# Kernel tuning notes

Hardware: AMD Instinct MI355X
Metric: run time of the kernel (lower is better)

The kernel has to match this reference:

```python
import jax, jax.numpy as jnp
import numpy as np

B, M, N, K = 2, 25000, 100000, 16
HID, DIM, NGROUPS = 64, 64, 8
GN_EPS = 1e-5


def conv1x1(x, w, b):
    # x: [B,C,M,K], w: [O,C], b: [O]
    return jnp.einsum('bcmk,oc->bomk', x, w) + b[None, :, None, None]


def group_norm(x, gamma, beta, ngroups):
    b, c, m, k = x.shape
    xg = x.reshape(b, ngroups, c // ngroups, m, k)
    mu = xg.mean(axis=(2, 3, 4), keepdims=True)
    var = xg.var(axis=(2, 3, 4), keepdims=True)
    xn = ((xg - mu) / jnp.sqrt(var + GN_EPS)).reshape(b, c, m, k)
    return xn * gamma[None, :, None, None] + beta[None, :, None, None]


def mlp(x, w1, b1, g, be, w2, b2):
    h = jax.nn.relu(group_norm(conv1x1(x, w1, b1), g, be, NGROUPS))
    return conv1x1(h, w2, b2)


def setup_inputs() -> dict:
    key = jax.random.key(0)
    ks = jax.random.split(key, 16)
    inp = {
        'q_xyzs': jax.random.normal(ks[0], (B, 3, M), jnp.float32),
        'k_xyzs': jax.random.normal(ks[1], (B, 3, N), jnp.float32),
        'knn_idx': jax.random.randint(ks[2], (B, M, K), 0, N),
        'mask': jax.random.randint(ks[3], (B, M, K), 0, 2).astype(bool),
        # embed_positions MLP params
        'pe_w1': jax.random.normal(ks[4], (HID, 4), jnp.float32) * 0.05,
        'pe_b1': jnp.zeros((HID,), jnp.float32),
        'pe_g': jnp.ones((HID,), jnp.float32),
        'pe_be': jnp.zeros((HID,), jnp.float32),
        'pe_w2': jax.random.normal(ks[5], (DIM, HID), jnp.float32) * 0.05,
        'pe_b2': jnp.zeros((DIM,), jnp.float32),
        # attention MLP params
        'at_w1': jax.random.normal(ks[6], (HID, DIM), jnp.float32) * 0.05,
        'at_b1': jnp.zeros((HID,), jnp.float32),
        'at_g': jnp.ones((HID,), jnp.float32),
        'at_be': jnp.zeros((HID,), jnp.float32),
        'at_w2': jax.random.normal(ks[7], (DIM, HID), jnp.float32) * 0.05,
        'at_b2': jnp.zeros((DIM,), jnp.float32),
    }
    return inp


def reference(q_xyzs, k_xyzs, knn_idx, mask,
              pe_w1, pe_b1, pe_g, pe_be, pe_w2, pe_b2,
              at_w1, at_b1, at_g, at_be, at_w2, at_b2):
    # gather KNN coordinates: [B,3,M,K]
    knn_xyzs = jax.vmap(lambda pts, idx: pts[:, idx])(k_xyzs, knn_idx)
    offset = knn_xyzs - q_xyzs[..., None]
    dist = jnp.linalg.norm(offset, axis=1, keepdims=True)  # [B,1,M,K]
    direction = offset / jnp.maximum(dist, 1e-12)
    local_pattern = jnp.concatenate([direction, dist], axis=1)  # [B,4,M,K]

    pe = mlp(local_pattern, pe_w1, pe_b1, pe_g, pe_be, pe_w2, pe_b2)  # [B,DIM,M,K]
    attn = mlp(pe, at_w1, at_b1, at_g, at_be, at_w2, at_b2)
    mask_value = -jnp.finfo(attn.dtype).max
    attn = jnp.where(mask[:, None], attn, mask_value)
    attn = jax.nn.softmax(attn, axis=-1)
    return (pe * attn).sum(axis=-1)  # [B,DIM,M]
```

## Files before the change

kernel.cpp:

```cpp
#include <hip/hip_runtime.h>

#define Bn 2
#define Mn 25000
#define Nn 100000
#define MK 400000
#define GN_EPS 1e-5f
#define NEG_BIG (-3.402823466e+38f)
#define LOG2E 1.44269504088896340736f
#define MASK_NEG (-60000.f)

#define G1 512
#define G2 512

#define BEFF_OFF 0
#define B1P_OFF  64
#define AB1P_OFF 192
#define AB2L_OFF 320
#define WF16_OFF 384
#define AW1P_OFF 6528
#define W1F_OFF  10624
#define MSK_OFF  11136
#define SP_OFF   36160
#define YP_OFF   52544
#define YS_OFF   183616
#define KXT_OFF  184128
#define QT_OFF   984128
#define XF_OFF   1184128

typedef _Float16 hf8 __attribute__((ext_vector_type(8)));
typedef _Float16 hf4 __attribute__((ext_vector_type(4)));
typedef _Float16 hf2 __attribute__((ext_vector_type(2)));
typedef float f32x16 __attribute__((ext_vector_type(16)));

__device__ __forceinline__ f32x16 mfma16(hf8 a, hf8 b, f32x16 c) {
    return __builtin_amdgcn_mfma_f32_32x32x16_f16(a, b, c, 0, 0, 0);
}
__device__ __forceinline__ f32x16 splat16(float v) {
    f32x16 x;
#pragma unroll
    for (int r = 0; r < 16; ++r) x[r] = v;
    return x;
}
__device__ __forceinline__ hf8 zero8() {
    hf8 z;
#pragma unroll
    for (int j = 0; j < 8; ++j) z[j] = (_Float16)0.f;
    return z;
}
__device__ __forceinline__ hf2 pkcvt(float a, float b) {
    return __builtin_bit_cast(hf2, __builtin_amdgcn_cvt_pkrtz(a, b));
}
__device__ __forceinline__ hf2 pkrelu(hf2 v) {
    hf2 z; z[0] = (_Float16)0.f; z[1] = (_Float16)0.f;
    return __builtin_elementwise_max(v, z);
}
__device__ __forceinline__ float waveSum(float v) {
#pragma unroll
    for (int s = 32; s; s >>= 1) v += __shfl_down(v, s, 64);
    return v;
}
#define ROWFN(r, lane) (((r) & 3) + 8*((r) >> 2) + 4*((lane) >> 5))
#define SWZH(row, col) ((col) ^ ((((row) & 7)) << 3))

__global__ __launch_bounds__(256) void prep0_kernel(
    const float* __restrict__ q, const float* __restrict__ kx,
    float* __restrict__ ws)
{
    float4* kxt = (float4*)(ws + KXT_OFF);
    float4* qt  = (float4*)(ws + QT_OFF);
    for (int e = blockIdx.x*256 + threadIdx.x; e < 2*Nn; e += gridDim.x*256) {
        const int b = e / Nn, n = e % Nn;
        float4 v;
        v.x = kx[(b*3+0)*Nn + n]; v.y = kx[(b*3+1)*Nn + n];
        v.z = kx[(b*3+2)*Nn + n]; v.w = 0.f;
        kxt[e] = v;
    }
    for (int e = blockIdx.x*256 + threadIdx.x; e < 2*Mn; e += gridDim.x*256) {
        const int b = e / Mn, m = e % Mn;
        float4 v;
        v.x = q[(b*3+0)*Mn + m]; v.y = q[(b*3+1)*Mn + m];
        v.z = q[(b*3+2)*Mn + m]; v.w = 0.f;
        qt[e] = v;
    }
}

__global__ __launch_bounds__(256) void gatherx_kernel(
    const int* __restrict__ idx, const int* __restrict__ mask,
    float* __restrict__ ws)
{
    __shared__ float red[4][16];
    const int b = blockIdx.y;
    const float4* kxt = (const float4*)(ws + KXT_OFF) + (size_t)b*Nn;
    const float4* qt  = (const float4*)(ws + QT_OFF)  + (size_t)b*Mn;
    _Float16* xf = (_Float16*)(ws + XF_OFF);
    unsigned short* m16 = (unsigned short*)(ws + MSK_OFF) + (size_t)b*25024;
    float v[14];
#pragma unroll
    for (int j = 0; j < 14; ++j) v[j] = 0.f;

    for (int i = blockIdx.x*256 + threadIdx.x; i < MK; i += G1*256) {
        const int mm = i >> 4;
        const int id = idx[(size_t)b*MK + i];
        const float4 kv = kxt[id];
        const float4 qv = qt[mm];
        const float ox = kv.x - qv.x, oy = kv.y - qv.y, oz = kv.z - qv.z;
        const float d  = sqrtf(ox*ox + oy*oy + oz*oz);
        const float inv = 1.0f / fmaxf(d, 1e-12f);
        const float x0 = ox*inv, x1 = oy*inv, x2 = oz*inv, x3 = d;

        const hf2 lo = pkcvt(x0, x1);
        const hf2 hi = pkcvt(x2, x3);
        hf4 pk;
        pk[0] = lo[0]; pk[1] = lo[1]; pk[2] = hi[0]; pk[3] = hi[1];
        *(hf4*)&xf[((size_t)b*MK + i)*4] = pk;

        const unsigned long long mb = __ballot(mask[(size_t)b*MK + i] != 0);
        if ((threadIdx.x & 63) == 0)
            *(unsigned long long*)&m16[i >> 4] = mb;

        v[0] += x0; v[1] += x1; v[2] += x2; v[3] += x3;
        v[4] += x0*x0; v[5] += x0*x1; v[6] += x0*x2; v[7] += x0*x3;
        v[8] += x1*x1; v[9] += x1*x2; v[10] += x1*x3;
        v[11] += x2*x2; v[12] += x2*x3; v[13] += x3*x3;
    }
    const int lane = threadIdx.x & 63, wv = threadIdx.x >> 6;
#pragma unroll
    for (int j = 0; j < 14; ++j) v[j] = waveSum(v[j]);
    if (lane == 0) {
#pragma unroll
        for (int j = 0; j < 14; ++j) red[wv][j] = v[j];
    }
    __syncthreads();
    if (threadIdx.x < 14)
        ws[SP_OFF + ((size_t)b*G1 + blockIdx.x)*16 + threadIdx.x] =
            red[0][threadIdx.x] + red[1][threadIdx.x] + red[2][threadIdx.x] + red[3][threadIdx.x];
}

__global__ void prep1_kernel(
    const float* __restrict__ ws_r,
    const float* __restrict__ w1, const float* __restrict__ b1,
    const float* __restrict__ g1, const float* __restrict__ be1,
    const float* __restrict__ w2, const float* __restrict__ pe_b2,
    const float* __restrict__ aw1, const float* __restrict__ ab1,
    const float* __restrict__ aw2, const float* __restrict__ ab2,
    float* __restrict__ ws)
{
    const int t = threadIdx.x;
    _Float16* WF = (_Float16*)(ws + WF16_OFF);

    if (blockIdx.x > 0) {
        const int e = (blockIdx.x - 1)*256 + t;
        const int o = e >> 6, c = e & 63;
        WF[e]        = (_Float16)w2[e];
        WF[4096 + e] = (_Float16)(aw2[e] * LOG2E);
        float acc = 0.f;
        for (int d = 0; d < 64; ++d) acc = fmaf(aw1[o*64 + d], w2[d*64 + c], acc);
        WF[8192 + e] = (_Float16)acc;
        return;
    }

    __shared__ double S[2][14];
    __shared__ double Sp[28][8];
    __shared__ float Eh[2][64], Eq[2][64];

    if (t < 224) {
        const int p = t >> 3, sub = t & 7;
        const int b = p / 14, j = p % 14;
        const float* src = ws_r + SP_OFF + (size_t)b*G1*16 + j;
        double acc = 0.0;
        for (int g = sub; g < G1; g += 8)
            acc += (double)src[(size_t)g*16];
        Sp[p][sub] = acc;
    }
    __syncthreads();
    if (t < 28) {
        double acc = 0.0;
#pragma unroll
        for (int s = 0; s < 8; ++s) acc += Sp[t][s];
        S[t / 14][t % 14] = acc;
    }
    __syncthreads();

    if (t < 128) {
        const int b = t >> 6, o = t & 63;
        const double inv = 1.0 / (double)MK;
        double mu[4];
#pragma unroll
        for (int c = 0; c < 4; ++c) mu[c] = S[b][c] * inv;
        double m2[4][4];
        {
            const int map[4][4] = {{0,1,2,3},{1,4,5,6},{2,5,7,8},{3,6,8,9}};
#pragma unroll
            for (int c = 0; c < 4; ++c)
#pragma unroll
                for (int c2 = 0; c2 < 4; ++c2)
                    m2[c][c2] = S[b][4 + map[c][c2]] * inv;
        }
        double w[4];
#pragma unroll
        for (int c = 0; c < 4; ++c) w[c] = (double)w1[o*4 + c];
        double s = 0.0, qd = 0.0;
#pragma unroll
        for (int c = 0; c < 4; ++c) {
            s += w[c] * mu[c];
#pragma unroll
            for (int c2 = 0; c2 < 4; ++c2) qd += w[c]*w[c2]*m2[c][c2];
        }
        const double bb = (double)b1[o];
        Eh[b][o] = (float)(s + bb);
        Eq[b][o] = (float)(qd + 2.0*bb*s + bb*bb);
    }
    __syncthreads();
    if (t < 128) {
        const int b = t >> 6, o = t & 63, g = o & ~7;
        float mg = 0.f, qg = 0.f;
#pragma unroll
        for (int j = 0; j < 8; ++j) { mg += Eh[b][g + j]; qg += Eq[b][g + j]; }
        mg *= 0.125f; qg *= 0.125f;
        const float var = fmaxf(qg - mg*mg, 0.f);
        const float a = g1[o] / sqrtf(var + GN_EPS);
        const float c1v = be1[o] - mg*a;
        _Float16* W1F = (_Float16*)(ws + W1F_OFF);
        hf8 wrow;
#pragma unroll
        for (int c = 0; c < 4; ++c) wrow[c] = (_Float16)(a * w1[o*4 + c]);
#pragma unroll
        for (int c = 4; c < 8; ++c) wrow[c] = (_Float16)0.f;
        *(hf8*)&W1F[(b*64 + o)*8] = wrow;
        ws[B1P_OFF + b*64 + o] = fmaf(a, b1[o], c1v);
    }
    if (t < 64) {
        float acc = ab1[t];
        for (int d = 0; d < 64; ++d) acc = fmaf(aw1[t*64 + d], pe_b2[d], acc);
        ws[BEFF_OFF + t] = acc;
    } else if (t < 128) {
        ws[AB2L_OFF + (t - 64)] = ab2[t - 64] * LOG2E;
    }
}

__global__ __launch_bounds__(256, 4) void pass2_kernel(
    const float* __restrict__ cws, float* __restrict__ ws)
{
    __shared__ __align__(16) _Float16 Xs[4][32][72];
    const int b = blockIdx.y;
    const int tid = threadIdx.x, lane = tid & 63, wv = tid >> 6;
    const int colA = lane & 31;
    const int klo = (lane >> 5) * 8;
    const _Float16* xf  = (const _Float16*)(cws + XF_OFF);
    const _Float16* WFe = (const _Float16*)(cws + WF16_OFF) + 8192;
    const _Float16* W1F = (const _Float16*)(cws + W1F_OFF);

    hf8 BW[2][4];
#pragma unroll
    for (int jc = 0; jc < 2; ++jc)
#pragma unroll
        for (int ks = 0; ks < 4; ++ks)
            BW[jc][ks] = *(const hf8*)&WFe[(2*colA + jc)*64 + 16*ks + klo];
    hf8 BX[2];
    if (klo == 0) {
        BX[0] = *(const hf8*)&W1F[(b*64 + 2*colA)*8];
        BX[1] = *(const hf8*)&W1F[(b*64 + 2*colA + 1)*8];
    } else { BX[0] = zero8(); BX[1] = zero8(); }
    const float bias0 = cws[B1P_OFF + b*64 + 2*colA];
    const float bias1 = cws[B1P_OFF + b*64 + 2*colA + 1];

    float sh[2] = {0.f, 0.f}, sq[2] = {0.f, 0.f};

    for (int base = blockIdx.x * 128; base < MK; base += G2 * 128) {
        const int pt0 = base + 32*wv;
        hf8 ax = zero8();
        if (klo == 0) {
            hf4 xv = *(const hf4*)&xf[((size_t)b*MK + pt0 + colA)*4];
#pragma unroll
            for (int j = 0; j < 4; ++j) ax[j] = xv[j];
        }
        f32x16 r0 = splat16(bias0), r1t = splat16(bias1);
        r0  = mfma16(ax, BX[0], r0);
        r1t = mfma16(ax, BX[1], r1t);
#pragma unroll
        for (int r = 0; r < 16; ++r) {
            const int row = ROWFN(r, lane);
            *(hf2*)&Xs[wv][row][2*colA] = pkrelu(pkcvt(r0[r], r1t[r]));
        }
        hf8 A[4];
#pragma unroll
        for (int ks = 0; ks < 4; ++ks)
            A[ks] = *(const hf8*)&Xs[wv][colA][16*ks + klo];
#pragma unroll
        for (int jc = 0; jc < 2; ++jc) {
            f32x16 C = splat16(0.f);
#pragma unroll
            for (int ks = 0; ks < 4; ++ks) C = mfma16(A[ks], BW[jc][ks], C);
#pragma unroll
            for (int r = 0; r < 16; ++r) {
                const float vy = C[r];
                sh[jc] += vy;
                sq[jc] = fmaf(vy, vy, sq[jc]);
            }
        }
    }

#pragma unroll
    for (int jc = 0; jc < 2; ++jc) {
        sh[jc] += __shfl_xor(sh[jc], 32, 64);
        sq[jc] += __shfl_xor(sq[jc], 32, 64);
    }
    __syncthreads();
    float* red = (float*)Xs;
    if (lane < 32) {
#pragma unroll
        for (int jc = 0; jc < 2; ++jc) {
            red[wv*128 +      2*colA + jc] = sh[jc];
            red[wv*128 + 64 + 2*colA + jc] = sq[jc];
        }
    }
    __syncthreads();
    if (tid < 128) {
        const float v = red[tid] + red[128 + tid] + red[256 + tid] + red[384 + tid];
        ws[YP_OFF + ((size_t)b*G2 + blockIdx.x)*128 + tid] = v;
    }
}

__global__ __launch_bounds__(64) void prep2a_kernel(
    const float* __restrict__ ws_r, float* __restrict__ ws)
{
    const int o2 = blockIdx.x;
    const int b = o2 >> 7, i = o2 & 127;
    const float* p = ws_r + YP_OFF + (size_t)b*G2*128 + i;
    double acc = 0.0;
    for (int g = threadIdx.x; g < G2; g += 64) acc += (double)p[(size_t)g*128];
#pragma unroll
    for (int s = 32; s; s >>= 1) acc += __shfl_down(acc, s, 64);
    if (threadIdx.x == 0) ((double*)(ws + YS_OFF))[o2] = acc;
}

__global__ void prep2b_kernel(const float* __restrict__ ws_r,
                              const float* __restrict__ g2, const float* __restrict__ be2,
                              const float* __restrict__ aw1, const float* __restrict__ ab1,
                              float* __restrict__ ws)
{
    __shared__ float EH[2][64], EQ[2][64];
    __shared__ float A2s[2][64];
    const int t = threadIdx.x;
    const double* YS = (const double*)(ws_r + YS_OFF);
    if (t < 128) {
        const int b = t >> 6, o = t & 63;
        const double invMK = 1.0 / (double)MK;
        const double my = YS[b*128 + o] * invMK;
        const double qy = YS[b*128 + 64 + o] * invMK;
        const double beff = (double)ws_r[BEFF_OFF + o];
        EH[b][o] = (float)(my + beff);
        EQ[b][o] = (float)(qy + 2.0*beff*my + beff*beff);
    }
    __syncthreads();
    if (t < 128) {
        const int b = t >> 6, o = t & 63, g = o & ~7;
        float mg = 0.f, qg = 0.f;
#pragma unroll
        for (int j = 0; j < 8; ++j) { mg += EH[b][g + j]; qg += EQ[b][g + j]; }
        mg *= 0.125f; qg *= 0.125f;
        const float var = fmaxf(qg - mg*mg, 0.f);
        const float a = g2[o] / sqrtf(var + GN_EPS);
        A2s[b][o] = a;
        ws[AB1P_OFF + b*64 + o] = fmaf(a, ab1[o], be2[o] - mg*a);
    }
    __syncthreads();
    _Float16* AW1P = (_Float16*)(ws + AW1P_OFF);
    for (int e = t; e < 8192; e += 256) {
        const int b = e >> 12, oc = e & 4095, o = oc >> 6;
        AW1P[e] = (_Float16)(A2s[b][o] * aw1[oc]);
    }
}

__global__ __launch_bounds__(256, 5) void pass3_kernel(
    const float* __restrict__ b2,
    const float* __restrict__ cws, float* __restrict__ out)
{
    __shared__ __align__(16) _Float16 Xs[8][32][64];
    float* O = (float*)Xs;

    const int b = blockIdx.y;
    const int base = blockIdx.x * 256;
    const int tid = threadIdx.x;
    const int lane = tid & 63, wv = tid >> 6;
    const int colA = lane & 31;
    const int hi = lane >> 5;
    const int klo = hi * 8;

    const _Float16* xf   = (const _Float16*)(cws + XF_OFF);
    const _Float16* WF   = (const _Float16*)(cws + WF16_OFF);
    const _Float16* AW1P = (const _Float16*)(cws + AW1P_OFF) + (size_t)b*4096;
    const _Float16* W1F  = (const _Float16*)(cws + W1F_OFF);
    const unsigned short* m16 = (const unsigned short*)(cws + MSK_OFF) + (size_t)b*25024;

    int pt0[2];
    pt0[0] = base + 64*wv;
    pt0[1] = base + 64*wv + 32;
    unsigned mb[2];
#pragma unroll
    for (int t = 0; t < 2; ++t)
        mb[t] = (pt0[t] < MK) ? *(const unsigned*)(m16 + (pt0[t] >> 4)) : 0u;
    const unsigned mbs0 = __builtin_amdgcn_readfirstlane(mb[0]);
    const unsigned mbs1 = __builtin_amdgcn_readfirstlane(mb[1]);

    {
        hf8 BX0, BX1;
        if (klo == 0) {
            BX0 = *(const hf8*)&W1F[(b*64 + 2*colA)*8];
            BX1 = *(const hf8*)&W1F[(b*64 + 2*colA + 1)*8];
        } else { BX0 = zero8(); BX1 = zero8(); }
        const float bias0 = cws[B1P_OFF + b*64 + 2*colA];
        const float bias1 = cws[B1P_OFF + b*64 + 2*colA + 1];
#pragma unroll
        for (int t = 0; t < 2; ++t) {
            hf8 ax = zero8();
            if (klo == 0 && pt0[t] < MK) {
                hf4 xv = *(const hf4*)&xf[((size_t)b*MK + pt0[t] + colA)*4];
#pragma unroll
                for (int j = 0; j < 4; ++j) ax[j] = xv[j];
            }
            f32x16 r0 = splat16(bias0), r1t = splat16(bias1);
            r0  = mfma16(ax, BX0, r0);
            r1t = mfma16(ax, BX1, r1t);
#pragma unroll
            for (int r = 0; r < 16; ++r) {
                const int row = ROWFN(r, lane);
                *(hf2*)&Xs[2*wv + t][row][SWZH(row, 2*colA)] = pkrelu(pkcvt(r0[r], r1t[r]));
            }
        }
    }

    hf2 pe_pk[2][16];
    {
        f32x16 p00 = splat16(b2[2*colA]);
        f32x16 p01 = splat16(b2[2*colA + 1]);
        f32x16 p10 = p00, p11 = p01;
#pragma unroll
        for (int ks = 0; ks < 4; ++ks) {
            const int off = SWZH(colA, 16*ks + klo);
            hf8 a0  = *(const hf8*)&Xs[2*wv    ][colA][off];
            hf8 a1  = *(const hf8*)&Xs[2*wv + 1][colA][off];
            hf8 b0f = *(const hf8*)&WF[(2*colA)*64 + 16*ks + klo];
            hf8 b1f = *(const hf8*)&WF[(2*colA + 1)*64 + 16*ks + klo];
            p00 = mfma16(a0, b0f, p00);
            p01 = mfma16(a0, b1f, p01);
            p10 = mfma16(a1, b0f, p10);
            p11 = mfma16(a1, b1f, p11);
        }
#pragma unroll
        for (int r = 0; r < 16; ++r) {
            const int row = ROWFN(r, lane);
            pe_pk[0][r] = pkcvt(p00[r], p01[r]);
            pe_pk[1][r] = pkcvt(p10[r], p11[r]);
            *(hf2*)&Xs[2*wv    ][row][SWZH(row, 2*colA)] = pe_pk[0][r];
            *(hf2*)&Xs[2*wv + 1][row][SWZH(row, 2*colA)] = pe_pk[1][r];
        }
    }

    {
        f32x16 h00 = splat16(cws[AB1P_OFF + b*64 + 2*colA]);
        f32x16 h01 = splat16(cws[AB1P_OFF + b*64 + 2*colA + 1]);
        f32x16 h10 = h00, h11 = h01;
#pragma unroll
        for (int ks = 0; ks < 4; ++ks) {
            const int off = SWZH(colA, 16*ks + klo);
            hf8 a0  = *(const hf8*)&Xs[2*wv    ][colA][off];
            hf8 a1  = *(const hf8*)&Xs[2*wv + 1][colA][off];
            hf8 b0f = *(const hf8*)&AW1P[(2*colA)*64 + 16*ks + klo];
            hf8 b1f = *(const hf8*)&AW1P[(2*colA + 1)*64 + 16*ks + klo];
            h00 = mfma16(a0, b0f, h00);
            h01 = mfma16(a0, b1f, h01);
            h10 = mfma16(a1, b0f, h10);
            h11 = mfma16(a1, b1f, h11);
        }
#pragma unroll
        for (int r = 0; r < 16; ++r) {
            const int row = ROWFN(r, lane);
            *(hf2*)&Xs[2*wv    ][row][SWZH(row, 2*colA)] = pkrelu(pkcvt(h00[r], h01[r]));
            *(hf2*)&Xs[2*wv + 1][row][SWZH(row, 2*colA)] = pkrelu(pkcvt(h10[r], h11[r]));
        }
    }

    f32x16 l00 = splat16(cws[AB2L_OFF + 2*colA]);
    f32x16 l01 = splat16(cws[AB2L_OFF + 2*colA + 1]);
    f32x16 l10 = l00, l11 = l01;
#pragma unroll
    for (int ks = 0; ks < 4; ++ks) {
        const int off = SWZH(colA, 16*ks + klo);
        hf8 a0  = *(const hf8*)&Xs[2*wv    ][colA][off];
        hf8 a1  = *(const hf8*)&Xs[2*wv + 1][colA][off];
        hf8 b0f = *(const hf8*)&WF[4096 + (2*colA)*64 + 16*ks + klo];
        hf8 b1f = *(const hf8*)&WF[4096 + (2*colA + 1)*64 + 16*ks + klo];
        l00 = mfma16(a0, b0f, l00);
        l01 = mfma16(a0, b1f, l01);
        l10 = mfma16(a1, b0f, l10);
        l11 = mfma16(a1, b1f, l11);
    }

    {
        const unsigned msh0 = mbs0 >> (4*hi);
        const unsigned msh1 = mbs1 >> (4*hi);
#pragma unroll
        for (int r = 0; r < 16; ++r) {
            const int bit = (r & 3) + 8*(r >> 2);
            const bool k0 = (msh0 >> bit) & 1u;
            const bool k1 = (msh1 >> bit) & 1u;
            l00[r] = k0 ? l00[r] : MASK_NEG;
            l01[r] = k0 ? l01[r] : MASK_NEG;
            l10[r] = k1 ? l10[r] : MASK_NEG;
            l11[r] = k1 ? l11[r] : MASK_NEG;
        }
    }

    __syncthreads();

    {
        auto softmax_tile = [&](const f32x16& lg, const hf2* pp, unsigned mbst,
                                int t, int j) {
#pragma unroll
            for (int mh = 0; mh < 2; ++mh) {
                float mx = lg[8*mh];
#pragma unroll
                for (int rr = 1; rr < 8; ++rr) mx = fmaxf(mx, lg[8*mh + rr]);
                mx = fmaxf(mx, __shfl_xor(mx, 32, 64));
                float se, sw = 0.f;
                if (((mbst >> (16*mh)) & 0xFFFFu) != 0u) {
                    se = 0.f;
#pragma unroll
                    for (int rr = 0; rr < 8; ++rr) {
                        const float e = exp2f(lg[8*mh + rr] - mx);
                        se += e;
                        sw = fmaf(e, (float)pp[8*mh + rr][j], sw);
                    }
                } else {
                    se = 8.f;
#pragma unroll
                    for (int rr = 0; rr < 8; ++rr) sw += (float)pp[8*mh + rr][j];
                }
                se += __shfl_xor(se, 32, 64);
                sw += __shfl_xor(sw, 32, 64);
                if (lane < 32)
                    O[(2*lane + j)*17 + (4*wv + 2*t + mh)] = sw * __builtin_amdgcn_rcpf(se);
            }
        };
        softmax_tile(l00, pe_pk[0], mbs0, 0, 0);
        softmax_tile(l01, pe_pk[0], mbs0, 0, 1);
        softmax_tile(l10, pe_pk[1], mbs1, 1, 0);
        softmax_tile(l11, pe_pk[1], mbs1, 1, 1);
    }
    __syncthreads();

    {
        const int o = tid >> 2, mq = (tid & 3) * 4;
        const int m0 = blockIdx.x * 16;
        if (m0 + mq < Mn) {
            float4 v;
            v.x = O[o*17 + mq];     v.y = O[o*17 + mq + 1];
            v.z = O[o*17 + mq + 2]; v.w = O[o*17 + mq + 3];
            *(float4*)&out[((size_t)b*64 + o)*Mn + m0 + mq] = v;
        }
    }
}

extern "C" void kernel_launch(void* const* d_in, const int* in_sizes, int n_in,
                              void* d_out, int out_size, void* d_ws, size_t ws_size,
                              hipStream_t stream) {
    (void)in_sizes; (void)n_in; (void)out_size; (void)ws_size;
    const float* q    = (const float*)d_in[0];
    const float* kx   = (const float*)d_in[1];
    const int*   idx  = (const int*)  d_in[2];
    const int*   mask = (const int*)  d_in[3];
    const float* w1   = (const float*)d_in[4];
    const float* b1   = (const float*)d_in[5];
    const float* g1   = (const float*)d_in[6];
    const float* be1  = (const float*)d_in[7];
    const float* w2   = (const float*)d_in[8];
    const float* b2   = (const float*)d_in[9];
    const float* aw1  = (const float*)d_in[10];
    const float* ab1  = (const float*)d_in[11];
    const float* g2   = (const float*)d_in[12];
    const float* be2  = (const float*)d_in[13];
    const float* aw2  = (const float*)d_in[14];
    const float* ab2  = (const float*)d_in[15];
    float* out = (float*)d_out;
    float* ws  = (float*)d_ws;

    prep0_kernel<<<256, 256, 0, stream>>>(q, kx, ws);
    gatherx_kernel<<<dim3(G1, Bn), 256, 0, stream>>>(idx, mask, ws);
    prep1_kernel<<<17, 256, 0, stream>>>(ws, w1, b1, g1, be1, w2, b2, aw1, ab1, aw2, ab2, ws);
    pass2_kernel<<<dim3(G2, Bn), 256, 0, stream>>>(ws, ws);
    prep2a_kernel<<<256, 64, 0, stream>>>(ws, ws);
    prep2b_kernel<<<1, 256, 0, stream>>>(ws, g2, be2, aw1, ab1, ws);
    pass3_kernel<<<dim3((MK + 255)/256, Bn), 256, 0, stream>>>(b2, ws, out);
}
```

Baseline: 220.8 us.

## Unroll gather loop by two, pad LDS rows instead of XOR swizzle

The gather kernel now processes two strided elements per iteration, loading both indices, masks and coordinate vectors before computing, to raise memory-level parallelism on the random kxt gather. In pass3, the XOR-swizzled LDS layout is replaced by padding each row to 72 halves, which simplifies address math. The launch-bounds minimum-blocks hint drops from 5 to 3, giving the compiler more registers per thread. The padding raises shared memory per block, and the lower occupancy hint may reduce latency hiding in pass3.

```diff
diff --git a/kernel.cpp b/kernel.cpp
--- a/kernel.cpp
+++ b/kernel.cpp
@@ -60,7 +60,6 @@
     return v;
 }
 #define ROWFN(r, lane) (((r) & 3) + 8*((r) >> 2) + 4*((lane) >> 5))
-#define SWZH(row, col) ((col) ^ ((((row) & 7)) << 3))
 
 __global__ __launch_bounds__(256) void prep0_kernel(
     const float* __restrict__ q, const float* __restrict__ kx,
@@ -98,23 +97,19 @@
 #pragma unroll
     for (int j = 0; j < 14; ++j) v[j] = 0.f;
 
-    for (int i = blockIdx.x*256 + threadIdx.x; i < MK; i += G1*256) {
-        const int mm = i >> 4;
-        const int id = idx[(size_t)b*MK + i];
-        const float4 kv = kxt[id];
-        const float4 qv = qt[mm];
+    auto process = [&](int i, const float4 kv, const float4 qv, int mk) {
         const float ox = kv.x - qv.x, oy = kv.y - qv.y, oz = kv.z - qv.z;
         const float d  = sqrtf(ox*ox + oy*oy + oz*oz);
         const float inv = 1.0f / fmaxf(d, 1e-12f);
         const float x0 = ox*inv, x1 = oy*inv, x2 = oz*inv, x3 = d;
 
         const hf2 lo = pkcvt(x0, x1);
-        const hf2 hi = pkcvt(x2, x3);
+        const hf2 h2 = pkcvt(x2, x3);
         hf4 pk;
-        pk[0] = lo[0]; pk[1] = lo[1]; pk[2] = hi[0]; pk[3] = hi[1];
+        pk[0] = lo[0]; pk[1] = lo[1]; pk[2] = h2[0]; pk[3] = h2[1];
         *(hf4*)&xf[((size_t)b*MK + i)*4] = pk;
 
-        const unsigned long long mb = __ballot(mask[(size_t)b*MK + i] != 0);
+        const unsigned long long mb = __ballot(mk != 0);
         if ((threadIdx.x & 63) == 0)
             *(unsigned long long*)&m16[i >> 4] = mb;
 
@@ -122,7 +117,31 @@
         v[4] += x0*x0; v[5] += x0*x1; v[6] += x0*x2; v[7] += x0*x3;
         v[8] += x1*x1; v[9] += x1*x2; v[10] += x1*x3;
         v[11] += x2*x2; v[12] += x2*x3; v[13] += x3*x3;
-    }
+    };
+
+    const int stride = G1*256;
+    int i = blockIdx.x*256 + threadIdx.x;
+    for (; i + stride < MK; i += 2*stride) {
+        const int iB = i + stride;
+        const int idA = idx[(size_t)b*MK + i];
+        const int idB = idx[(size_t)b*MK + iB];
+        const int mA  = mask[(size_t)b*MK + i];
+        const int mB  = mask[(size_t)b*MK + iB];
+        const float4 kvA = kxt[idA];
+        const float4 kvB = kxt[idB];
+        const float4 qvA = qt[i >> 4];
+        const float4 qvB = qt[iB >> 4];
+        process(i,  kvA, qvA, mA);
+        process(iB, kvB, qvB, mB);
+    }
+    for (; i < MK; i += stride) {
+        const int id = idx[(size_t)b*MK + i];
+        const int mk = mask[(size_t)b*MK + i];
+        const float4 kv = kxt[id];
+        const float4 qv = qt[i >> 4];
+        process(i, kv, qv, mk);
+    }
+
     const int lane = threadIdx.x & 63, wv = threadIdx.x >> 6;
 #pragma unroll
     for (int j = 0; j < 14; ++j) v[j] = waveSum(v[j]);
@@ -372,11 +391,11 @@
     }
 }
 
-__global__ __launch_bounds__(256, 5) void pass3_kernel(
+__global__ __launch_bounds__(256, 3) void pass3_kernel(
     const float* __restrict__ b2,
     const float* __restrict__ cws, float* __restrict__ out)
 {
-    __shared__ __align__(16) _Float16 Xs[8][32][64];
+    __shared__ __align__(16) _Float16 Xs[8][32][72];
     float* O = (float*)Xs;
 
     const int b = blockIdx.y;
@@ -425,7 +444,7 @@
 #pragma unroll
             for (int r = 0; r < 16; ++r) {
                 const int row = ROWFN(r, lane);
-                *(hf2*)&Xs[2*wv + t][row][SWZH(row, 2*colA)] = pkrelu(pkcvt(r0[r], r1t[r]));
+                *(hf2*)&Xs[2*wv + t][row][2*colA] = pkrelu(pkcvt(r0[r], r1t[r]));
             }
         }
     }
@@ -437,11 +456,11 @@
         f32x16 p10 = p00, p11 = p01;
 #pragma unroll
         for (int ks = 0; ks < 4; ++ks) {
-            const int off = SWZH(colA, 16*ks + klo);
+            const int off = 16*ks + klo;
             hf8 a0  = *(const hf8*)&Xs[2*wv    ][colA][off];
             hf8 a1  = *(const hf8*)&Xs[2*wv + 1][colA][off];
-            hf8 b0f = *(const hf8*)&WF[(2*colA)*64 + 16*ks + klo];
-            hf8 b1f = *(const hf8*)&WF[(2*colA + 1)*64 + 16*ks + klo];
+            hf8 b0f = *(const hf8*)&WF[(2*colA)*64 + off];
+            hf8 b1f = *(const hf8*)&WF[(2*colA + 1)*64 + off];
             p00 = mfma16(a0, b0f, p00);
             p01 = mfma16(a0, b1f, p01);
             p10 = mfma16(a1, b0f, p10);
@@ -452,8 +471,8 @@
             const int row = ROWFN(r, lane);
             pe_pk[0][r] = pkcvt(p00[r], p01[r]);
             pe_pk[1][r] = pkcvt(p10[r], p11[r]);
-            *(hf2*)&Xs[2*wv    ][row][SWZH(row, 2*colA)] = pe_pk[0][r];
-            *(hf2*)&Xs[2*wv + 1][row][SWZH(row, 2*colA)] = pe_pk[1][r];
+            *(hf2*)&Xs[2*wv    ][row][2*colA] = pe_pk[0][r];
+            *(hf2*)&Xs[2*wv + 1][row][2*colA] = pe_pk[1][r];
         }
     }
 
@@ -463,11 +482,11 @@
         f32x16 h10 = h00, h11 = h01;
 #pragma unroll
         for (int ks = 0; ks < 4; ++ks) {
-            const int off = SWZH(colA, 16*ks + klo);
+            const int off = 16*ks + klo;
             hf8 a0  = *(const hf8*)&Xs[2*wv    ][colA][off];
             hf8 a1  = *(const hf8*)&Xs[2*wv + 1][colA][off];
-            hf8 b0f = *(const hf8*)&AW1P[(2*colA)*64 + 16*ks + klo];
-            hf8 b1f = *(const hf8*)&AW1P[(2*colA + 1)*64 + 16*ks + klo];
+            hf8 b0f = *(const hf8*)&AW1P[(2*colA)*64 + off];
+            hf8 b1f = *(const hf8*)&AW1P[(2*colA + 1)*64 + off];
             h00 = mfma16(a0, b0f, h00);
             h01 = mfma16(a0, b1f, h01);
             h10 = mfma16(a1, b0f, h10);
@@ -476,8 +495,8 @@
 #pragma unroll
         for (int r = 0; r < 16; ++r) {
             const int row = ROWFN(r, lane);
-            *(hf2*)&Xs[2*wv    ][row][SWZH(row, 2*colA)] = pkrelu(pkcvt(h00[r], h01[r]));
-            *(hf2*)&Xs[2*wv + 1][row][SWZH(row, 2*colA)] = pkrelu(pkcvt(h10[r], h11[r]));
+            *(hf2*)&Xs[2*wv    ][row][2*colA] = pkrelu(pkcvt(h00[r], h01[r]));
+            *(hf2*)&Xs[2*wv + 1][row][2*colA] = pkrelu(pkcvt(h10[r], h11[r]));
         }
     }
 
@@ -486,11 +505,11 @@
     f32x16 l10 = l00, l11 = l01;
 #pragma unroll
     for (int ks = 0; ks < 4; ++ks) {
-        const int off = SWZH(colA, 16*ks + klo);
+        const int off = 16*ks + klo;
         hf8 a0  = *(const hf8*)&Xs[2*wv    ][colA][off];
         hf8 a1  = *(const hf8*)&Xs[2*wv + 1][colA][off];
-        hf8 b0f = *(const hf8*)&WF[4096 + (2*colA)*64 + 16*ks + klo];
-        hf8 b1f = *(const hf8*)&WF[4096 + (2*colA + 1)*64 + 16*ks + klo];
+        hf8 b0f = *(const hf8*)&WF[4096 + (2*colA)*64 + off];
+        hf8 b1f = *(const hf8*)&WF[4096 + (2*colA + 1)*64 + off];
         l00 = mfma16(a0, b0f, l00);
         l01 = mfma16(a0, b1f, l01);
         l10 = mfma16(a1, b0f, l10);
```

Result: faster. 201.3 us (-8.8%).
